# Kernel tuning notes

Hardware: AMD Instinct MI355X
Metric: run time of the kernel (lower is better)

## Reference

```python
import math
import jax, jax.numpy as jnp
import numpy as np


def _unfold(x, kh, kw, dh, dw, ph, pw):
    """F.unfold equivalent: returns (n, c, kh*kw, h, w), channel-major like torch."""
    n, c, h, w = x.shape
    xp = jnp.pad(x, ((0, 0), (0, 0), (ph, ph), (pw, pw)))
    patches = jnp.stack(
        [xp[:, :, i * dh:i * dh + h, j * dw:j * dw + w]
         for i in range(kh) for j in range(kw)],
        axis=2,
    )
    return patches  # (n, c, kh*kw, h, w)


def setup_inputs() -> dict:
    key = jax.random.key(0)
    k1, k2, k3, k4 = jax.random.split(key, 4)
    n, c, h, w = 8, 128, 64, 64
    x = jax.random.normal(k1, (n, c, h, w), dtype=jnp.float32)
    p1_w = 0.1 * jax.random.normal(k2, (1, c, h, 1), dtype=jnp.float32)  # trunc_normal std=0.1
    p7_w = jax.random.normal(k3, (c, c), dtype=jnp.float32) / np.sqrt(c)  # 1x1 conv c->c
    # grouped 1x1 conv: groups=4, out=c*21, weight (c*21, c//4)
    p10_w = jax.random.normal(k4, (c * 21, c // 4), dtype=jnp.float32) / np.sqrt(c // 4)
    return {"x": x, "p1_w": p1_w, "p7_w": p7_w, "p10_w": p10_w}


def reference(x, p1_w, p7_w, p10_w):
    n, c, h, w = x.shape
    g = 4
    t1 = p1_w * x                        # (n,c,h,w)
    t2 = x + t1
    t4 = jax.nn.relu(x)
    t5 = _unfold(x, 3, 7, 1, 1, 1, 3)    # (n,c,21,h,w)
    t7 = jnp.einsum('oc,nchw->nohw', p7_w, t4)        # 1x1 conv
    t8 = _unfold(t7, 1, 5, 1, 3, 0, 6)   # (n,c,5,h,w)
    t9 = x[:, :, None] - t8              # (n,c,5,h,w)
    # grouped 1x1 conv c -> c*21, groups=4
    xg = t2.reshape(n, g, c // g, h, w)
    wg = p10_w.reshape(g, (c * 21) // g, c // g)
    t10 = jnp.einsum('ngihw,goi->ngohw', xg, wg).reshape(n, c * 21, h, w)
    # score: (n,c,hw) x (n,hw,c*21) -> (n,c,c*21)
    t1f = t1.reshape(n, c, h * w)
    t5f = t5.reshape(n, c * 21, h * w)
    t11 = jnp.einsum('nck,nmk->ncm', t1f, t5f) / math.sqrt(h * w)
    t12 = t9.mean(2)                     # (n,c,h,w)
    t13 = jnp.einsum('ncm,nmk->nck', t11, t10.reshape(n, c * 21, h * w))
    t13 = t13.reshape(n, c, h, w) / math.sqrt(c * 21)
    return jnp.maximum(t13, t12)
```

## Files before the change

### kernel.cpp

```cpp
#include <hip/hip_runtime.h>
#include <hip/hip_bf16.h>

typedef unsigned short ushort_t;
typedef unsigned int uint_t;
typedef __attribute__((ext_vector_type(8))) short s16x8;
typedef __attribute__((ext_vector_type(4))) float f32x4;
typedef __attribute__((ext_vector_type(4))) ushort_t u16x4;
typedef __attribute__((ext_vector_type(8))) ushort_t u16x8;

__device__ __forceinline__ ushort_t f2bf(float f) {
    uint_t u = __float_as_uint(f);
    uint_t r = (u + 0x7FFFu + ((u >> 16) & 1u)) >> 16;
    return (ushort_t)r;
}
__device__ __forceinline__ float bf2f(ushort_t u) {
    return __uint_as_float(((uint_t)u) << 16);
}
__device__ __forceinline__ s16x8 relu8(s16x8 v) {
    s16x8 r;
#pragma unroll
    for (int e = 0; e < 8; ++e) { short xv = v[e]; r[e] = (xv < 0) ? (short)0 : xv; }
    return r;
}

__global__ __launch_bounds__(256) void prep_all(const float* __restrict__ x,
                                                const float* __restrict__ p1,
                                                const float* __restrict__ p10,
                                                const float* __restrict__ p7,
                                                ushort_t* __restrict__ t1h,
                                                ushort_t* __restrict__ xpTh,
                                                ushort_t* __restrict__ wfc,
                                                ushort_t* __restrict__ p7h) {
    __shared__ float xs[64][65];
    __shared__ float p1s[64];
    const int b = blockIdx.x;
    const int t = threadIdx.x;
    if (b < 1024) {
        const int y  = b & 63;
        const int c0 = ((b >> 6) & 1) * 64;
        const int n  = b >> 7;
        if (t < 64) p1s[t] = p1[(c0 + t) * 64 + y];
#pragma unroll
        for (int cc = 0; cc < 4; ++cc) {
            int c = cc * 16 + (t >> 4);
            int px = (t & 15) * 4;
            float4 v = *(const float4*)(x + ((size_t)((n * 128 + c0 + c)) * 64 + y) * 64 + px);
            xs[c][px] = v.x; xs[c][px + 1] = v.y; xs[c][px + 2] = v.z; xs[c][px + 3] = v.w;
        }
        __syncthreads();
        {
            int c = t >> 2, px0 = (t & 3) * 16;
            float pv = p1s[c];
            u16x8 o0, o1;
#pragma unroll
            for (int e = 0; e < 8; ++e) {
                o0[e] = f2bf(pv * xs[c][px0 + e]);
                o1[e] = f2bf(pv * xs[c][px0 + 8 + e]);
            }
            ushort_t* dst = t1h + (size_t)(n * 128 + c0 + c) * 4096 + y * 64 + px0;
            *(u16x8*)dst = o0;
            *(u16x8*)(dst + 8) = o1;
        }
        {
            int p = t >> 2, cx0 = (t & 3) * 16;
            u16x8 r0, r1;
#pragma unroll
            for (int e = 0; e < 8; ++e) {
                r0[e] = f2bf(xs[cx0 + e][p]);
                r1[e] = f2bf(xs[cx0 + 8 + e][p]);
            }
            size_t baseP = ((size_t)n * 4752 + (y + 1) * 72 + p + 3) * 128 + c0 + cx0;
            *(u16x8*)(xpTh + baseP) = r0;
            *(u16x8*)(xpTh + baseP + 8) = r1;
        }
    } else {
        int idx = (b - 1024) * 256 + t;
        if (idx < 83968) {
            int chunk = idx & 15;
            int rest  = idx >> 4;
            int n = rest / 656;
            int s = rest - n * 656;
            int yy, xx;
            if (s < 144) { yy = (s < 72) ? 0 : 65; xx = s % 72; }
            else { int s2 = s - 144; yy = (s2 >> 3) + 1; int k = s2 & 7; xx = (k < 3) ? k : k + 64; }
            u16x8 z = {};
            *(u16x8*)(xpTh + ((size_t)n * 4752 + yy * 72 + xx) * 128 + chunk * 8) = z;
        } else if (idx < 83968 + 86016) {
            int i = idx - 83968;
            int c32 = i & 31;
            int j = (i >> 5) & 31;
            int rest = i >> 10;
            int tap = rest % 21, g = rest / 21;
            wfc[i] = f2bf(p10[((32 * g + c32) * 21 + tap) * 32 + j]);
        } else if (idx < 83968 + 86016 + 16384) {
            int i = idx - 83968 - 86016;
            p7h[i] = f2bf(p7[i]);
        }
    }
}

__global__ __launch_bounds__(256) void guf_mfma(const ushort_t* __restrict__ xpTh,
                                                const ushort_t* __restrict__ wfc,
                                                const ushort_t* __restrict__ t1h,
                                                ushort_t* __restrict__ uparth) {
    __shared__ ushort_t Ts[6 * 72 * 32];
    __shared__ ushort_t Gs[32 * 256];
    const int pt = blockIdx.x;
    const int p0 = pt * 256;
    const int g  = blockIdx.y;
    const int n  = blockIdx.z;
    const int tid = threadIdx.x;
    const int lane = tid & 63, wid = tid >> 6;
    const int q = lane >> 4, fr = lane & 15;
    const int y0 = p0 >> 6;

    const ushort_t* src = xpTh + ((size_t)n * 4752 + y0 * 72) * 128 + g * 32;
    for (int flat = tid; flat < 1728; flat += 256) {
        int qq = flat & 3;
        int cc = (flat >> 2) % 72;
        int rr = (flat >> 2) / 72;
        u16x8 v = *(const u16x8*)(src + ((size_t)rr * 72 + cc) * 128 + qq * 8);
        *(u16x8*)&Ts[(rr * 72 + cc) * 32 + ((qq ^ ((cc >> 1) & 3)) * 8)] = v;
    }
    __syncthreads();

    const ushort_t* wbase = wfc + (size_t)g * 21 * 1024 + fr * 32 + q * 8;
    f32x4 acc[2][4] = {};
    for (int tap = 0; tap < 21; ++tap) {
        const int ki = tap / 7, kj = tap - ki * 7;
        s16x8 a[2], b[4];
#pragma unroll
        for (int i = 0; i < 2; ++i)
            a[i] = *(const s16x8*)(wbase + tap * 1024 + i * 16 * 32);
#pragma unroll
        for (int jj = 0; jj < 4; ++jj) {
            int col = wid * 64 + jj * 16 + fr;
            int rr = (col >> 6) + ki;
            int cc = (col & 63) + kj;
            b[jj] = *(const s16x8*)&Ts[(rr * 72 + cc) * 32 + ((q ^ ((cc >> 1) & 3)) * 8)];
        }
#pragma unroll
        for (int i = 0; i < 2; ++i)
#pragma unroll
            for (int jj = 0; jj < 4; ++jj)
                acc[i][jj] = __builtin_amdgcn_mfma_f32_16x16x32_bf16(a[i], b[jj], acc[i][jj], 0, 0, 0);
    }
#pragma unroll
    for (int i = 0; i < 2; ++i) {
#pragma unroll
        for (int jj = 0; jj < 4; ++jj) {
            int p = wid * 64 + jj * 16 + fr;
            int pc = p >> 3, pe = p & 7;
#pragma unroll
            for (int reg = 0; reg < 4; ++reg) {
                int j = i * 16 + q * 4 + reg;
                Gs[j * 256 + ((pc ^ (j & 7)) * 8) + pe] = f2bf(acc[i][jj][reg]);
            }
        }
    }
    __syncthreads();

    const ushort_t* t1base = t1h + (size_t)n * 128 * 4096 + p0;
    const int cb = wid * 32;
    f32x4 accu[2][2] = {};
    for (int kk = 0; kk < 8; ++kk) {
        s16x8 a[2], b[2];
#pragma unroll
        for (int i = 0; i < 2; ++i) {
            int j = i * 16 + fr;
            a[i] = *(const s16x8*)&Gs[j * 256 + (((kk * 4 + q) ^ (j & 7)) * 8)];
        }
#pragma unroll
        for (int l = 0; l < 2; ++l)
            b[l] = *(const s16x8*)(t1base + (size_t)(cb + l * 16 + fr) * 4096 + kk * 32 + q * 8);
#pragma unroll
        for (int i = 0; i < 2; ++i)
#pragma unroll
            for (int l = 0; l < 2; ++l)
                accu[i][l] = __builtin_amdgcn_mfma_f32_16x16x32_bf16(a[i], b[l], accu[i][l], 0, 0, 0);
    }
#pragma unroll
    for (int i = 0; i < 2; ++i) {
#pragma unroll
        for (int l = 0; l < 2; ++l) {
            int c = cb + l * 16 + fr;
            u16x4 o;
#pragma unroll
            for (int reg = 0; reg < 4; ++reg) o[reg] = f2bf(accu[i][l][reg]);
            *(u16x4*)&uparth[((size_t)(n * 16 + pt) * 128 + c) * 128 + g * 32 + i * 16 + q * 4] = o;
        }
    }
}

__global__ void ureduce_kernel(const ushort_t* __restrict__ uparth, ushort_t* __restrict__ Uh) {
    int idx = blockIdx.x * 256 + threadIdx.x;
    int n = idx >> 14, rc = idx & 16383;
    float s = 0.0f;
#pragma unroll
    for (int k = 0; k < 16; ++k) s += bf2f(uparth[(size_t)((n * 16 + k) << 14) + rc]);
    Uh[idx] = f2bf(s * 0.015625f);
}

__global__ __launch_bounds__(256) void outf_mfma(const ushort_t* __restrict__ p7h,
                                                 const ushort_t* __restrict__ xpTh,
                                                 const ushort_t* __restrict__ Uh,
                                                 const float* __restrict__ p1,
                                                 float* __restrict__ out) {
    __shared__ ushort_t Bs[8192];
    __shared__ ushort_t Cs[9984];
    __shared__ ushort_t T12s[8192];
    __shared__ float p1s[128];
    const int y = blockIdx.x;
    const int n = blockIdx.y;
    const int tid = threadIdx.x;
    const int lane = tid & 63, w = tid >> 6;
    const int q = lane >> 4, fr = lane & 15;

    if (tid < 128) p1s[tid] = p1[tid * 64 + y];
    int adS[4], chS[4];
#pragma unroll
    for (int it = 0; it < 4; ++it) {
        int slot = it * 256 + tid;
        int row = slot >> 4, ch = slot & 15;
        chS[it] = ch;
        adS[it] = (row * 16 + (ch ^ (row & 15))) * 8;
        u16x8 v = *(const u16x8*)(xpTh + ((size_t)n * 4752 + (y + 1) * 72 + 3 + row) * 128 + ch * 8);
        *(u16x8*)&Bs[adS[it]] = v;
    }
    __syncthreads();

    f32x4 acc[2][4] = {};
    for (int ks = 0; ks < 4; ++ks) {
        s16x8 a[2], b[4];
#pragma unroll
        for (int i = 0; i < 2; ++i)
            a[i] = *(const s16x8*)(p7h + (w * 32 + i * 16 + fr) * 128 + ks * 32 + q * 8);
#pragma unroll
        for (int jj = 0; jj < 4; ++jj) {
            int rb = jj * 16 + fr;
            b[jj] = relu8(*(const s16x8*)&Bs[(rb * 16 + ((ks * 4 + q) ^ (rb & 15))) * 8]);
        }
#pragma unroll
        for (int i = 0; i < 2; ++i)
#pragma unroll
            for (int jj = 0; jj < 4; ++jj)
                acc[i][jj] = __builtin_amdgcn_mfma_f32_16x16x32_bf16(a[i], b[jj], acc[i][jj], 0, 0, 0);
    }
    for (int i2 = tid; i2 < 4992; i2 += 256) ((uint_t*)Cs)[i2] = 0u;
    __syncthreads();
#pragma unroll
    for (int i = 0; i < 2; ++i)
#pragma unroll
        for (int jj = 0; jj < 4; ++jj) {
            int col = jj * 16 + fr;
#pragma unroll
            for (int reg = 0; reg < 4; ++reg) {
                int row = w * 32 + i * 16 + q * 4 + reg;
                Cs[row * 78 + 6 + col] = f2bf(acc[i][jj][reg]);
            }
        }
    __syncthreads();
    for (int rep = 0; rep < 32; ++rep) {
        int flat = rep * 256 + tid;
        int c = flat >> 6, xx = flat & 63;
        float s = 0.0f;
#pragma unroll
        for (int jj = 0; jj < 5; ++jj)
            s += bf2f(Cs[c * 78 + xx + 3 * jj]);
        float xv = bf2f(Bs[(xx * 16 + ((c >> 3) ^ (xx & 15))) * 8 + (c & 7)]);
        T12s[flat] = f2bf(xv - 0.2f * s);
    }
    __syncthreads();
#pragma unroll
    for (int it = 0; it < 4; ++it) {
        u16x8 v = *(u16x8*)&Bs[adS[it]];
        u16x8 o;
#pragma unroll
        for (int e = 0; e < 8; ++e)
            o[e] = f2bf(bf2f(v[e]) * (1.0f + p1s[chS[it] * 8 + e]));
        *(u16x8*)&Bs[adS[it]] = o;
    }
    __syncthreads();
    f32x4 acc2[2][4] = {};
    for (int ks = 0; ks < 4; ++ks) {
        s16x8 a[2], b[4];
#pragma unroll
        for (int i = 0; i < 2; ++i)
            a[i] = *(const s16x8*)(Uh + ((size_t)(n * 128 + w * 32 + i * 16 + fr)) * 128 + ks * 32 + q * 8);
#pragma unroll
        for (int jj = 0; jj < 4; ++jj) {
            int rb = jj * 16 + fr;
            b[jj] = *(const s16x8*)&Bs[(rb * 16 + ((ks * 4 + q) ^ (rb & 15))) * 8];
        }
#pragma unroll
        for (int i = 0; i < 2; ++i)
#pragma unroll
            for (int jj = 0; jj < 4; ++jj)
                acc2[i][jj] = __builtin_amdgcn_mfma_f32_16x16x32_bf16(a[i], b[jj], acc2[i][jj], 0, 0, 0);
    }
    const float scale = 0.0192879257f;
#pragma unroll
    for (int i = 0; i < 2; ++i)
#pragma unroll
        for (int jj = 0; jj < 4; ++jj) {
            int col = jj * 16 + fr;
#pragma unroll
            for (int reg = 0; reg < 4; ++reg) {
                int row = w * 32 + i * 16 + q * 4 + reg;
                size_t oi = ((size_t)(n * 128 + row)) * 4096 + y * 64 + col;
                out[oi] = fmaxf(bf2f(T12s[row * 64 + col]), acc2[i][jj][reg] * scale);
            }
        }
}

extern "C" void kernel_launch(void* const* d_in, const int* in_sizes, int n_in,
                              void* d_out, int out_size, void* d_ws, size_t ws_size,
                              hipStream_t stream) {
    const float* x   = (const float*)d_in[0];
    const float* p1  = (const float*)d_in[1];
    const float* p7  = (const float*)d_in[2];
    const float* p10 = (const float*)d_in[3];
    float* out = (float*)d_out;

    ushort_t* t1h    = (ushort_t*)d_ws;
    ushort_t* xpTh   = t1h + 4194304;
    ushort_t* p7h    = xpTh + 4866048;
    ushort_t* wfc    = p7h + 16384;
    ushort_t* Uh     = wfc + 86016;
    ushort_t* uparth = Uh + 131072;

    prep_all<<<1752, 256, 0, stream>>>(x, p1, p10, p7, t1h, xpTh, wfc, p7h);
    guf_mfma<<<dim3(16, 4, 8), 256, 0, stream>>>(xpTh, wfc, t1h, uparth);
    ureduce_kernel<<<512, 256, 0, stream>>>(uparth, Uh);
    outf_mfma<<<dim3(64, 8), 256, 0, stream>>>(p7h, xpTh, Uh, p1, out);
}
```

Measured before the change: 45.71 us.

## Halve per-block work in guf and outf kernels to double grid parallelism

The guf_mfma kernel now processes 128 pixels per block instead of 256, which doubles its grid to 1024 blocks and makes the ureduce step sum 32 partials instead of 16. The outf_mfma kernel is split over output channels into two halves of 64, giving 1024 blocks with smaller LDS use. This targets under-occupancy on a GPU with many CUs (grids of 512 blocks). In exchange, the reduction traffic grows, the uparth workspace doubles in size, and outf duplicates the input load and the shifted-sum setup across both channel halves.

```diff
diff --git a/kernel.cpp b/kernel.cpp
--- a/kernel.cpp
+++ b/kernel.cpp
@@ -103,10 +103,10 @@
                                                 const ushort_t* __restrict__ wfc,
                                                 const ushort_t* __restrict__ t1h,
                                                 ushort_t* __restrict__ uparth) {
-    __shared__ ushort_t Ts[6 * 72 * 32];
-    __shared__ ushort_t Gs[32 * 256];
+    __shared__ ushort_t Ts[4 * 72 * 32];
+    __shared__ ushort_t Gs[32 * 128];
     const int pt = blockIdx.x;
-    const int p0 = pt * 256;
+    const int p0 = pt * 128;
     const int g  = blockIdx.y;
     const int n  = blockIdx.z;
     const int tid = threadIdx.x;
@@ -115,7 +115,7 @@
     const int y0 = p0 >> 6;
 
     const ushort_t* src = xpTh + ((size_t)n * 4752 + y0 * 72) * 128 + g * 32;
-    for (int flat = tid; flat < 1728; flat += 256) {
+    for (int flat = tid; flat < 1152; flat += 256) {
         int qq = flat & 3;
         int cc = (flat >> 2) % 72;
         int rr = (flat >> 2) / 72;
@@ -125,16 +125,16 @@
     __syncthreads();
 
     const ushort_t* wbase = wfc + (size_t)g * 21 * 1024 + fr * 32 + q * 8;
-    f32x4 acc[2][4] = {};
+    f32x4 acc[2][2] = {};
     for (int tap = 0; tap < 21; ++tap) {
         const int ki = tap / 7, kj = tap - ki * 7;
-        s16x8 a[2], b[4];
+        s16x8 a[2], b[2];
 #pragma unroll
         for (int i = 0; i < 2; ++i)
             a[i] = *(const s16x8*)(wbase + tap * 1024 + i * 16 * 32);
 #pragma unroll
-        for (int jj = 0; jj < 4; ++jj) {
-            int col = wid * 64 + jj * 16 + fr;
+        for (int jj = 0; jj < 2; ++jj) {
+            int col = wid * 32 + jj * 16 + fr;
             int rr = (col >> 6) + ki;
             int cc = (col & 63) + kj;
             b[jj] = *(const s16x8*)&Ts[(rr * 72 + cc) * 32 + ((q ^ ((cc >> 1) & 3)) * 8)];
@@ -142,19 +142,19 @@
 #pragma unroll
         for (int i = 0; i < 2; ++i)
 #pragma unroll
-            for (int jj = 0; jj < 4; ++jj)
+            for (int jj = 0; jj < 2; ++jj)
                 acc[i][jj] = __builtin_amdgcn_mfma_f32_16x16x32_bf16(a[i], b[jj], acc[i][jj], 0, 0, 0);
     }
 #pragma unroll
     for (int i = 0; i < 2; ++i) {
 #pragma unroll
-        for (int jj = 0; jj < 4; ++jj) {
-            int p = wid * 64 + jj * 16 + fr;
+        for (int jj = 0; jj < 2; ++jj) {
+            int p = wid * 32 + jj * 16 + fr;
             int pc = p >> 3, pe = p & 7;
 #pragma unroll
             for (int reg = 0; reg < 4; ++reg) {
                 int j = i * 16 + q * 4 + reg;
-                Gs[j * 256 + ((pc ^ (j & 7)) * 8) + pe] = f2bf(acc[i][jj][reg]);
+                Gs[j * 128 + ((pc ^ (j & 7)) * 8) + pe] = f2bf(acc[i][jj][reg]);
             }
         }
     }
@@ -163,12 +163,12 @@
     const ushort_t* t1base = t1h + (size_t)n * 128 * 4096 + p0;
     const int cb = wid * 32;
     f32x4 accu[2][2] = {};
-    for (int kk = 0; kk < 8; ++kk) {
+    for (int kk = 0; kk < 4; ++kk) {
         s16x8 a[2], b[2];
 #pragma unroll
         for (int i = 0; i < 2; ++i) {
             int j = i * 16 + fr;
-            a[i] = *(const s16x8*)&Gs[j * 256 + (((kk * 4 + q) ^ (j & 7)) * 8)];
+            a[i] = *(const s16x8*)&Gs[j * 128 + (((kk * 4 + q) ^ (j & 7)) * 8)];
         }
 #pragma unroll
         for (int l = 0; l < 2; ++l)
@@ -187,7 +187,7 @@
             u16x4 o;
 #pragma unroll
             for (int reg = 0; reg < 4; ++reg) o[reg] = f2bf(accu[i][l][reg]);
-            *(u16x4*)&uparth[((size_t)(n * 16 + pt) * 128 + c) * 128 + g * 32 + i * 16 + q * 4] = o;
+            *(u16x4*)&uparth[((size_t)(n * 32 + pt) * 128 + c) * 128 + g * 32 + i * 16 + q * 4] = o;
         }
     }
 }
@@ -197,7 +197,7 @@
     int n = idx >> 14, rc = idx & 16383;
     float s = 0.0f;
 #pragma unroll
-    for (int k = 0; k < 16; ++k) s += bf2f(uparth[(size_t)((n * 16 + k) << 14) + rc]);
+    for (int k = 0; k < 32; ++k) s += bf2f(uparth[(size_t)((n * 32 + k) << 14) + rc]);
     Uh[idx] = f2bf(s * 0.015625f);
 }
 
@@ -207,11 +207,12 @@
                                                  const float* __restrict__ p1,
                                                  float* __restrict__ out) {
     __shared__ ushort_t Bs[8192];
-    __shared__ ushort_t Cs[9984];
-    __shared__ ushort_t T12s[8192];
+    __shared__ ushort_t Cs[4992];
+    __shared__ ushort_t T12s[4096];
     __shared__ float p1s[128];
-    const int y = blockIdx.x;
-    const int n = blockIdx.y;
+    const int y  = blockIdx.x;
+    const int mh = blockIdx.y;
+    const int n  = blockIdx.z;
     const int tid = threadIdx.x;
     const int lane = tid & 63, w = tid >> 6;
     const int q = lane >> 4, fr = lane & 15;
@@ -229,45 +230,40 @@
     }
     __syncthreads();
 
-    f32x4 acc[2][4] = {};
+    f32x4 acc[4] = {};
     for (int ks = 0; ks < 4; ++ks) {
-        s16x8 a[2], b[4];
-#pragma unroll
-        for (int i = 0; i < 2; ++i)
-            a[i] = *(const s16x8*)(p7h + (w * 32 + i * 16 + fr) * 128 + ks * 32 + q * 8);
+        s16x8 a = *(const s16x8*)(p7h + (mh * 64 + w * 16 + fr) * 128 + ks * 32 + q * 8);
+        s16x8 b[4];
 #pragma unroll
         for (int jj = 0; jj < 4; ++jj) {
             int rb = jj * 16 + fr;
             b[jj] = relu8(*(const s16x8*)&Bs[(rb * 16 + ((ks * 4 + q) ^ (rb & 15))) * 8]);
         }
 #pragma unroll
-        for (int i = 0; i < 2; ++i)
-#pragma unroll
-            for (int jj = 0; jj < 4; ++jj)
-                acc[i][jj] = __builtin_amdgcn_mfma_f32_16x16x32_bf16(a[i], b[jj], acc[i][jj], 0, 0, 0);
-    }
-    for (int i2 = tid; i2 < 4992; i2 += 256) ((uint_t*)Cs)[i2] = 0u;
-    __syncthreads();
-#pragma unroll
-    for (int i = 0; i < 2; ++i)
-#pragma unroll
-        for (int jj = 0; jj < 4; ++jj) {
-            int col = jj * 16 + fr;
-#pragma unroll
-            for (int reg = 0; reg < 4; ++reg) {
-                int row = w * 32 + i * 16 + q * 4 + reg;
-                Cs[row * 78 + 6 + col] = f2bf(acc[i][jj][reg]);
-            }
-        }
-    __syncthreads();
-    for (int rep = 0; rep < 32; ++rep) {
+        for (int jj = 0; jj < 4; ++jj)
+            acc[jj] = __builtin_amdgcn_mfma_f32_16x16x32_bf16(a, b[jj], acc[jj], 0, 0, 0);
+    }
+    for (int i2 = tid; i2 < 2496; i2 += 256) ((uint_t*)Cs)[i2] = 0u;
+    __syncthreads();
+#pragma unroll
+    for (int jj = 0; jj < 4; ++jj) {
+        int col = jj * 16 + fr;
+#pragma unroll
+        for (int reg = 0; reg < 4; ++reg) {
+            int row = w * 16 + q * 4 + reg;
+            Cs[row * 78 + 6 + col] = f2bf(acc[jj][reg]);
+        }
+    }
+    __syncthreads();
+    for (int rep = 0; rep < 16; ++rep) {
         int flat = rep * 256 + tid;
-        int c = flat >> 6, xx = flat & 63;
+        int cl = flat >> 6, xx = flat & 63;
         float s = 0.0f;
 #pragma unroll
         for (int jj = 0; jj < 5; ++jj)
-            s += bf2f(Cs[c * 78 + xx + 3 * jj]);
-        float xv = bf2f(Bs[(xx * 16 + ((c >> 3) ^ (xx & 15))) * 8 + (c & 7)]);
+            s += bf2f(Cs[cl * 78 + xx + 3 * jj]);
+        int cg = mh * 64 + cl;
+        float xv = bf2f(Bs[(xx * 16 + ((cg >> 3) ^ (xx & 15))) * 8 + (cg & 7)]);
         T12s[flat] = f2bf(xv - 0.2f * s);
     }
     __syncthreads();
@@ -281,36 +277,30 @@
         *(u16x8*)&Bs[adS[it]] = o;
     }
     __syncthreads();
-    f32x4 acc2[2][4] = {};
+    f32x4 acc2[4] = {};
     for (int ks = 0; ks < 4; ++ks) {
-        s16x8 a[2], b[4];
-#pragma unroll
-        for (int i = 0; i < 2; ++i)
-            a[i] = *(const s16x8*)(Uh + ((size_t)(n * 128 + w * 32 + i * 16 + fr)) * 128 + ks * 32 + q * 8);
+        s16x8 a = *(const s16x8*)(Uh + ((size_t)(n * 128 + mh * 64 + w * 16 + fr)) * 128 + ks * 32 + q * 8);
+        s16x8 b[4];
 #pragma unroll
         for (int jj = 0; jj < 4; ++jj) {
             int rb = jj * 16 + fr;
             b[jj] = *(const s16x8*)&Bs[(rb * 16 + ((ks * 4 + q) ^ (rb & 15))) * 8];
         }
 #pragma unroll
-        for (int i = 0; i < 2; ++i)
-#pragma unroll
-            for (int jj = 0; jj < 4; ++jj)
-                acc2[i][jj] = __builtin_amdgcn_mfma_f32_16x16x32_bf16(a[i], b[jj], acc2[i][jj], 0, 0, 0);
+        for (int jj = 0; jj < 4; ++jj)
+            acc2[jj] = __builtin_amdgcn_mfma_f32_16x16x32_bf16(a, b[jj], acc2[jj], 0, 0, 0);
     }
     const float scale = 0.0192879257f;
 #pragma unroll
-    for (int i = 0; i < 2; ++i)
-#pragma unroll
-        for (int jj = 0; jj < 4; ++jj) {
-            int col = jj * 16 + fr;
-#pragma unroll
-            for (int reg = 0; reg < 4; ++reg) {
-                int row = w * 32 + i * 16 + q * 4 + reg;
-                size_t oi = ((size_t)(n * 128 + row)) * 4096 + y * 64 + col;
-                out[oi] = fmaxf(bf2f(T12s[row * 64 + col]), acc2[i][jj][reg] * scale);
-            }
-        }
+    for (int jj = 0; jj < 4; ++jj) {
+        int col = jj * 16 + fr;
+#pragma unroll
+        for (int reg = 0; reg < 4; ++reg) {
+            int rl = w * 16 + q * 4 + reg;
+            size_t oi = ((size_t)(n * 128 + mh * 64 + rl)) * 4096 + y * 64 + col;
+            out[oi] = fmaxf(bf2f(T12s[rl * 64 + col]), acc2[jj][reg] * scale);
+        }
+    }
 }
 
 extern "C" void kernel_launch(void* const* d_in, const int* in_sizes, int n_in,
@@ -330,7 +320,7 @@
     ushort_t* uparth = Uh + 131072;
 
     prep_all<<<1752, 256, 0, stream>>>(x, p1, p10, p7, t1h, xpTh, wfc, p7h);
-    guf_mfma<<<dim3(16, 4, 8), 256, 0, stream>>>(xpTh, wfc, t1h, uparth);
+    guf_mfma<<<dim3(32, 4, 8), 256, 0, stream>>>(xpTh, wfc, t1h, uparth);
     ureduce_kernel<<<512, 256, 0, stream>>>(uparth, Uh);
-    outf_mfma<<<dim3(64, 8), 256, 0, stream>>>(p7h, xpTh, Uh, p1, out);
-}
+    outf_mfma<<<dim3(64, 2, 8), 256, 0, stream>>>(p7h, xpTh, Uh, p1, out);
+}
```

Result: slower. 48.56 us (+6.2%).
